# Performance work log

Measured on AMD Instinct MI355X. Metric: run time of the kernel, lower is better.

## Reference

```python
import jax, jax.numpy as jnp
import numpy as np

IN_FEATURES_LS = (64, 128, 256, 512)
OUT_FEATURES = 1024
MAX_FEAT = max(IN_FEATURES_LS)
N_TOKENS = 65536


def setup_inputs() -> dict:
    key = jax.random.key(0)
    kx, kg, kw, kb = jax.random.split(key, 4)
    x = jax.random.normal(kx, (N_TOKENS, MAX_FEAT), dtype=jnp.float32)
    gidx = jax.random.randint(kg, (N_TOKENS,), 0, len(IN_FEATURES_LS))
    # per-sample declared input size; values are exactly entries of IN_FEATURES_LS
    in_feat_size = jnp.asarray(IN_FEATURES_LS, dtype=jnp.int64 if jax.config.jax_enable_x64 else jnp.int32)[gidx]
    weight = jax.random.normal(kw, (len(IN_FEATURES_LS), OUT_FEATURES, MAX_FEAT), dtype=jnp.float32) * 0.02
    bias = jax.random.normal(kb, (len(IN_FEATURES_LS), OUT_FEATURES), dtype=jnp.float32) * 0.02
    return {"x": x, "in_feat_size": in_feat_size, "weight": weight, "bias": bias}


def reference(x, in_feat_size, weight, bias):
    # mask[g, i] = i < in_features_ls[g]; zero out padded weight columns
    sizes = jnp.asarray(IN_FEATURES_LS, dtype=jnp.int32)
    feat_mask = (jnp.arange(MAX_FEAT)[None, :] < sizes[:, None]).astype(x.dtype)  # [G, max_feat]
    out = jnp.zeros(x.shape[:-1] + (OUT_FEATURES,), dtype=x.dtype)
    for idx, feat_size in enumerate(IN_FEATURES_LS):
        w = weight[idx] * feat_mask[idx][None, :]          # [out, max_feat]
        y = jnp.einsum('oi,ni->no', w, x) + bias[idx]       # [N, out]
        sel = (in_feat_size == feat_size).astype(x.dtype)[..., None]
        out = out + sel * y
    return out
```

## Files before the change

### kernel.cpp

```cpp
#include <hip/hip_runtime.h>
#include <hip/hip_bf16.h>

#define N_TOKENS 65536
#define MAXF 512
#define OUTF 1024
#define NGROUP 4

typedef __attribute__((ext_vector_type(8))) short short8;
typedef __attribute__((ext_vector_type(4))) float floatx4;
typedef unsigned short ushort_t;
typedef unsigned int uint_t;

__device__ __forceinline__ uint_t f2bf(float f) {
    uint_t u = __float_as_uint(f);
    u += 0x7fffu + ((u >> 16) & 1u);
    return u >> 16;
}

#define OFF_BASES  0
#define OFF_BHIST  4096
#define OFF_BSTART 8192
#define OFF_LISTS  16384
#define OFF_XB     (1u<<20)
#define OFF_WB     ((1u<<20) + ((size_t)N_TOKENS*MAXF*2))
#define WS_FULL    (OFF_WB + (size_t)NGROUP*OUTF*MAXF*2)
#define WS_MIN     (OFF_LISTS + (size_t)N_TOKENS*4)

__constant__ int c_wstart[4] = {0, 65536, 196608, 458752};

__global__ void hist_kernel(const int* __restrict__ sizes, int* __restrict__ blockHist) {
    __shared__ int h[4][NGROUP];
    int t = threadIdx.x, wave = t >> 6;
    int tok = blockIdx.x * 256 + t;
    int g = __ffs(sizes[tok]) - 7;
    #pragma unroll
    for (int gg = 0; gg < NGROUP; ++gg) {
        unsigned long long m = __ballot(g == gg);
        if ((t & 63) == 0) h[wave][gg] = __popcll(m);
    }
    __syncthreads();
    if (t < NGROUP)
        blockHist[blockIdx.x * NGROUP + t] = h[0][t] + h[1][t] + h[2][t] + h[3][t];
}

__global__ void scan_kernel(const int* __restrict__ blockHist,
                            int* __restrict__ blockStart, int* __restrict__ bases) {
    __shared__ int4 sh[256];
    int t = threadIdx.x;
    int4 v = ((const int4*)blockHist)[t];
    sh[t] = v;
    __syncthreads();
    for (int d = 1; d < 256; d <<= 1) {
        int4 u = sh[t];
        int4 a = make_int4(0, 0, 0, 0);
        if (t >= d) a = sh[t - d];
        __syncthreads();
        u.x += a.x; u.y += a.y; u.z += a.z; u.w += a.w;
        sh[t] = u;
        __syncthreads();
    }
    int4 incl = sh[t];
    int4 tot = sh[255];
    int b0 = 0, b1 = tot.x, b2 = b1 + tot.y, b3 = b2 + tot.z, b4 = b3 + tot.w;
    blockStart[t * 4 + 0] = b0 + incl.x - v.x;
    blockStart[t * 4 + 1] = b1 + incl.y - v.y;
    blockStart[t * 4 + 2] = b2 + incl.z - v.z;
    blockStart[t * 4 + 3] = b3 + incl.w - v.w;
    if (t == 0) {
        bases[0] = b0; bases[1] = b1; bases[2] = b2; bases[3] = b3; bases[4] = b4;
    }
}

__global__ void scatter_kernel(const int* __restrict__ sizes,
                               const int* __restrict__ blockStart,
                               int* __restrict__ lists) {
    __shared__ int wcnt[4][NGROUP];
    int t = threadIdx.x, wave = t >> 6, lane = t & 63;
    int tok = blockIdx.x * 256 + t;
    int g = __ffs(sizes[tok]) - 7;
    int pos = 0;
    #pragma unroll
    for (int gg = 0; gg < NGROUP; ++gg) {
        unsigned long long m = __ballot(g == gg);
        if (g == gg) pos = __popcll(m & ((1ull << lane) - 1ull));
        if (lane == 0) wcnt[wave][gg] = __popcll(m);
    }
    __syncthreads();
    int off = blockStart[blockIdx.x * 4 + g];
    for (int w = 0; w < wave; ++w) off += wcnt[w][g];
    lists[off + pos] = tok;
}

__global__ void convx_kernel(const float* __restrict__ x, const int* __restrict__ bases,
                             const int* __restrict__ lists, ushort_t* __restrict__ xb) {
    int c0 = bases[1] - bases[0], c1 = bases[2] - bases[1],
        c2 = bases[3] - bases[2], c3 = bases[4] - bases[3];
    int p1 = c0 << 3;
    int p2 = p1 + (c1 << 4);
    int p3 = p2 + (c2 << 5);
    int T  = p3 + (c3 << 6);
    int xs1 = c0 << 6;
    int xs2 = xs1 + (c1 << 7);
    int xs3 = xs2 + (c2 << 8);
    int stride = gridDim.x * blockDim.x;
    for (int id = blockIdx.x * blockDim.x + threadIdx.x; id < T; id += stride) {
        int g, local, base, xs;
        if (id < p1)      { g = 0; local = id;      base = bases[0]; xs = 0;   }
        else if (id < p2) { g = 1; local = id - p1; base = bases[1]; xs = xs1; }
        else if (id < p3) { g = 2; local = id - p2; base = bases[2]; xs = xs2; }
        else              { g = 3; local = id - p3; base = bases[3]; xs = xs3; }
        int shift = 3 + g;
        int sl = local >> shift;
        int k  = (local - (sl << shift)) << 3;
        int tok = lists[base + sl];
        const floatx4* src = (const floatx4*)(x + (size_t)tok * MAXF + k);
        floatx4 a = src[0], b = src[1];
        short8 v;
        v[0] = (short)f2bf(a[0]); v[1] = (short)f2bf(a[1]);
        v[2] = (short)f2bf(a[2]); v[3] = (short)f2bf(a[3]);
        v[4] = (short)f2bf(b[0]); v[5] = (short)f2bf(b[1]);
        v[6] = (short)f2bf(b[2]); v[7] = (short)f2bf(b[3]);
        *(short8*)(xb + (size_t)xs + ((size_t)sl << (6 + g)) + k) = v;
    }
}

__global__ void convw_kernel(const float* __restrict__ weight, ushort_t* __restrict__ wb) {
    int id = blockIdx.x * 256 + threadIdx.x;
    int g, local, ws;
    if (id < 8192)       { g = 0; local = id;         ws = 0;      }
    else if (id < 24576) { g = 1; local = id - 8192;  ws = 65536;  }
    else if (id < 57344) { g = 2; local = id - 24576; ws = 196608; }
    else                 { g = 3; local = id - 57344; ws = 458752; }
    int shift = 3 + g;
    int row = local >> shift;
    int k = (local - (row << shift)) << 3;
    const floatx4* src = (const floatx4*)(weight + (size_t)g * OUTF * MAXF + (size_t)row * MAXF + k);
    floatx4 a = src[0], b = src[1];
    short8 v;
    v[0] = (short)f2bf(a[0]); v[1] = (short)f2bf(a[1]);
    v[2] = (short)f2bf(a[2]); v[3] = (short)f2bf(a[3]);
    v[4] = (short)f2bf(b[0]); v[5] = (short)f2bf(b[1]);
    v[6] = (short)f2bf(b[2]); v[7] = (short)f2bf(b[3]);
    *(short8*)(wb + ws + ((size_t)row << (6 + g)) + k) = v;
}

#define GLOAD_LDS16(gptr, lptr)                                                \
    __builtin_amdgcn_global_load_lds(                                          \
        (const __attribute__((address_space(1))) uint_t*)(gptr),               \
        (__attribute__((address_space(3))) uint_t*)(lptr), 16, 0, 0)

__global__ __launch_bounds__(512, 1) void gemm_bf16_kernel(
    const ushort_t* __restrict__ xb, const ushort_t* __restrict__ wb,
    const float* __restrict__ bias, const int* __restrict__ bases,
    const int* __restrict__ lists, float* __restrict__ out) {

    const int c0 = bases[1] - bases[0], c1 = bases[2] - bases[1],
              c2 = bases[3] - bases[2], c3 = bases[4] - bases[3];
    const int t0 = ((c0 + 255) >> 8) << 2;
    const int t1 = ((c1 + 255) >> 8) << 2;
    const int t2 = ((c2 + 255) >> 8) << 2;
    const int t3 = ((c3 + 255) >> 8) << 2;
    const int xs1 = c0 << 6;
    const int xs2 = xs1 + (c1 << 7);
    const int xs3 = xs2 + (c2 << 8);

    int id = blockIdx.x;
    int g, local, count, gbase, xs, wsb;
    if (id < t0)                { g = 0; local = id;                count = c0; gbase = bases[0]; xs = 0;   wsb = 0;      }
    else if (id < t0 + t1)      { g = 1; local = id - t0;           count = c1; gbase = bases[1]; xs = xs1; wsb = 65536;  }
    else if (id < t0 + t1 + t2) { g = 2; local = id - t0 - t1;      count = c2; gbase = bases[2]; xs = xs2; wsb = 196608; }
    else if (id < t0 + t1 + t2 + t3)
                                { g = 3; local = id - t0 - t1 - t2; count = c3; gbase = bases[3]; xs = xs3; wsb = 458752; }
    else return;

    const int mt = local >> 2, nt = local & 3;
    const int m_base = mt << 8;
    const int n_base = nt << 8;
    const int K_log = 6 + g;
    const int nsteps = 1 << (g + 1);
    const int rows = min(256, count - m_base);

    __shared__ ushort_t As[2][256 * 32];
    __shared__ ushort_t Bs[2][256 * 32];

    const int t = threadIdx.x;
    const int wave = t >> 6, lane = t & 63;
    const int wm = wave >> 2, wn = wave & 3;
    const int quad = lane >> 4, l16 = lane & 15;
    const int rsub = lane >> 2;
    const int kq   = (lane & 3) * 8;

    const ushort_t* aptr[2];
    const ushort_t* bptr[2];
    #pragma unroll
    for (int j = 0; j < 2; ++j) {
        int br = wave * 32 + j * 16;
        int ar = min(m_base + br + rsub, count - 1);
        aptr[j] = xb + (size_t)xs + ((size_t)ar << K_log) + kq;
        int nr = n_base + br + rsub;
        bptr[j] = wb + (size_t)wsb + ((size_t)nr << K_log) + kq;
    }

    floatx4 acc[8][4];
    #pragma unroll
    for (int i = 0; i < 8; ++i)
        #pragma unroll
        for (int j = 0; j < 4; ++j) acc[i][j] = (floatx4)(0.0f);

    #pragma unroll
    for (int j = 0; j < 2; ++j) {
        int br = wave * 32 + j * 16;
        GLOAD_LDS16(aptr[j], &As[0][br * 32]);
        GLOAD_LDS16(bptr[j], &Bs[0][br * 32]);
    }
    __syncthreads();

    int buf = 0;
    for (int s = 0; s < nsteps; ++s) {
        if (s + 1 < nsteps) {
            int k0 = (s + 1) << 5;
            #pragma unroll
            for (int j = 0; j < 2; ++j) {
                int br = wave * 32 + j * 16;
                GLOAD_LDS16(aptr[j] + k0, &As[buf ^ 1][br * 32]);
                GLOAD_LDS16(bptr[j] + k0, &Bs[buf ^ 1][br * 32]);
            }
        }
        short8 af[8], bf[4];
        #pragma unroll
        for (int mi = 0; mi < 8; ++mi)
            af[mi] = *(const short8*)&As[buf][(wm * 128 + mi * 16 + l16) * 32 + quad * 8];
        #pragma unroll
        for (int ni = 0; ni < 4; ++ni)
            bf[ni] = *(const short8*)&Bs[buf][(wn * 64 + ni * 16 + l16) * 32 + quad * 8];
        #pragma unroll
        for (int mi = 0; mi < 8; ++mi)
            #pragma unroll
            for (int ni = 0; ni < 4; ++ni)
                acc[mi][ni] = __builtin_amdgcn_mfma_f32_16x16x32_bf16(
                    af[mi], bf[ni], acc[mi][ni], 0, 0, 0);
        __syncthreads();
        buf ^= 1;
    }

    #pragma unroll
    for (int ni = 0; ni < 4; ++ni) {
        int col = n_base + wn * 64 + ni * 16 + l16;
        float bv = bias[g * OUTF + col];
        #pragma unroll
        for (int mi = 0; mi < 8; ++mi) {
            int mloc = wm * 128 + mi * 16 + quad * 4;
            #pragma unroll
            for (int r = 0; r < 4; ++r) {
                int m = mloc + r;
                if (m < rows) {
                    int tok = lists[gbase + m_base + m];
                    out[(size_t)tok * OUTF + col] = acc[mi][ni][r] + bv;
                }
            }
        }
    }
}

__global__ __launch_bounds__(256) void gemm_fp32_kernel(
    const float* __restrict__ x, const float* __restrict__ weight,
    const float* __restrict__ bias, const int* __restrict__ bases,
    const int* __restrict__ lists, float* __restrict__ out) {

    const int g = blockIdx.z;
    const int gbase = bases[g];
    const int count = bases[g + 1] - gbase;
    const int m_base = blockIdx.y * 128;
    if (m_base >= count) return;
    const int n_base = blockIdx.x * 128;
    const int K = 64 << g;
    const int rows = min(128, count - m_base);

    __shared__ ushort_t As[128][40];
    __shared__ ushort_t Bs[128][40];
    __shared__ int idxs[128];

    const int t = threadIdx.x;
    if (t < 128) idxs[t] = (t < rows) ? lists[gbase + m_base + t] : lists[gbase + m_base];
    __syncthreads();

    const int wave = t >> 6, lane = t & 63;
    const int wm = wave >> 1, wn = wave & 1;
    const int quad = lane >> 4, l16 = lane & 15;

    floatx4 acc[4][4];
    #pragma unroll
    for (int i = 0; i < 4; ++i)
        #pragma unroll
        for (int j = 0; j < 4; ++j) acc[i][j] = (floatx4)(0.0f);

    const float* wg = weight + (size_t)g * OUTF * MAXF;

    for (int k0 = 0; k0 < K; k0 += 32) {
        #pragma unroll
        for (int rep = 0; rep < 4; ++rep) {
            int id = t + rep * 256;
            int row = id >> 3;
            int kqq = id & 7;
            floatx4 av = *(const floatx4*)(x + (size_t)idxs[row] * MAXF + k0 + kqq * 4);
            unsigned long long pa = (unsigned long long)f2bf(av[0]) |
                ((unsigned long long)f2bf(av[1]) << 16) |
                ((unsigned long long)f2bf(av[2]) << 32) |
                ((unsigned long long)f2bf(av[3]) << 48);
            *(unsigned long long*)&As[row][kqq * 4] = pa;
            floatx4 bvv = *(const floatx4*)(wg + (size_t)(n_base + row) * MAXF + k0 + kqq * 4);
            unsigned long long pb = (unsigned long long)f2bf(bvv[0]) |
                ((unsigned long long)f2bf(bvv[1]) << 16) |
                ((unsigned long long)f2bf(bvv[2]) << 32) |
                ((unsigned long long)f2bf(bvv[3]) << 48);
            *(unsigned long long*)&Bs[row][kqq * 4] = pb;
        }
        __syncthreads();

        short8 af[4], bf[4];
        #pragma unroll
        for (int mi = 0; mi < 4; ++mi)
            af[mi] = *(const short8*)&As[wm * 64 + mi * 16 + l16][quad * 8];
        #pragma unroll
        for (int ni = 0; ni < 4; ++ni)
            bf[ni] = *(const short8*)&Bs[wn * 64 + ni * 16 + l16][quad * 8];
        #pragma unroll
        for (int mi = 0; mi < 4; ++mi)
            #pragma unroll
            for (int ni = 0; ni < 4; ++ni)
                acc[mi][ni] = __builtin_amdgcn_mfma_f32_16x16x32_bf16(
                    af[mi], bf[ni], acc[mi][ni], 0, 0, 0);
        __syncthreads();
    }

    #pragma unroll
    for (int ni = 0; ni < 4; ++ni) {
        int col = n_base + wn * 64 + ni * 16 + l16;
        float bv = bias[g * OUTF + col];
        #pragma unroll
        for (int mi = 0; mi < 4; ++mi) {
            int mloc = wm * 64 + mi * 16 + quad * 4;
            #pragma unroll
            for (int r = 0; r < 4; ++r) {
                int m = mloc + r;
                if (m < rows)
                    out[(size_t)idxs[m] * OUTF + col] = acc[mi][ni][r] + bv;
            }
        }
    }
}

extern "C" void kernel_launch(void* const* d_in, const int* in_sizes, int n_in,
                              void* d_out, int out_size, void* d_ws, size_t ws_size,
                              hipStream_t stream) {
    const float* x      = (const float*)d_in[0];
    const int*   sizes  = (const int*)d_in[1];
    const float* weight = (const float*)d_in[2];
    const float* bias   = (const float*)d_in[3];
    float* out = (float*)d_out;

    char* ws = (char*)d_ws;
    int* bases      = (int*)(ws + OFF_BASES);
    int* blockHist  = (int*)(ws + OFF_BHIST);
    int* blockStart = (int*)(ws + OFF_BSTART);
    int* lists      = (int*)(ws + OFF_LISTS);
    ushort_t* xb    = (ushort_t*)(ws + OFF_XB);
    ushort_t* wb    = (ushort_t*)(ws + OFF_WB);

    hist_kernel<<<N_TOKENS / 256, 256, 0, stream>>>(sizes, blockHist);
    scan_kernel<<<1, 256, 0, stream>>>(blockHist, blockStart, bases);
    scatter_kernel<<<N_TOKENS / 256, 256, 0, stream>>>(sizes, blockStart, lists);

    if (ws_size >= WS_FULL) {
        convw_kernel<<<480, 256, 0, stream>>>(weight, wb);
        convx_kernel<<<2048, 256, 0, stream>>>(x, bases, lists, xb);
        gemm_bf16_kernel<<<1036, 512, 0, stream>>>(xb, wb, bias, bases, lists, out);
    } else {
        dim3 grid(OUTF / 128, N_TOKENS / 128, NGROUP);
        gemm_fp32_kernel<<<grid, 256, 0, stream>>>(x, weight, bias, bases, lists, out);
    }
}
```

Before: 484.5 us.

## Merge prep kernels, fuse conversions, triple-buffer GEMM with swizzled LDS

Replaces the histogram/scan/scatter chain with one atomic-based prep kernel that writes per-group token lists at fixed offsets. The two bf16 conversion kernels become one launch. The GEMM gets a three-stage LDS ring in dynamic shared memory with explicit vmcnt waits and one barrier per step, an XOR swizzle on the LDS column to cut bank conflicts, and output token indices cached in LDS. The goal is fewer launches and better overlap of loads with MFMA, at the cost of nondeterministic list order and more shared memory per block.

```diff
diff --git a/kernel.cpp b/kernel.cpp
--- a/kernel.cpp
+++ b/kernel.cpp
@@ -17,64 +17,17 @@
     return u >> 16;
 }
 
-#define OFF_BASES  0
-#define OFF_BHIST  4096
-#define OFF_BSTART 8192
+#define OFF_CNT    0
 #define OFF_LISTS  16384
-#define OFF_XB     (1u<<20)
-#define OFF_WB     ((1u<<20) + ((size_t)N_TOKENS*MAXF*2))
+#define OFF_XB     (2u<<20)
+#define OFF_WB     ((2u<<20) + ((size_t)N_TOKENS*MAXF*2))
 #define WS_FULL    (OFF_WB + (size_t)NGROUP*OUTF*MAXF*2)
-#define WS_MIN     (OFF_LISTS + (size_t)N_TOKENS*4)
-
-__constant__ int c_wstart[4] = {0, 65536, 196608, 458752};
-
-__global__ void hist_kernel(const int* __restrict__ sizes, int* __restrict__ blockHist) {
-    __shared__ int h[4][NGROUP];
-    int t = threadIdx.x, wave = t >> 6;
-    int tok = blockIdx.x * 256 + t;
-    int g = __ffs(sizes[tok]) - 7;
-    #pragma unroll
-    for (int gg = 0; gg < NGROUP; ++gg) {
-        unsigned long long m = __ballot(g == gg);
-        if ((t & 63) == 0) h[wave][gg] = __popcll(m);
-    }
-    __syncthreads();
-    if (t < NGROUP)
-        blockHist[blockIdx.x * NGROUP + t] = h[0][t] + h[1][t] + h[2][t] + h[3][t];
-}
-
-__global__ void scan_kernel(const int* __restrict__ blockHist,
-                            int* __restrict__ blockStart, int* __restrict__ bases) {
-    __shared__ int4 sh[256];
-    int t = threadIdx.x;
-    int4 v = ((const int4*)blockHist)[t];
-    sh[t] = v;
-    __syncthreads();
-    for (int d = 1; d < 256; d <<= 1) {
-        int4 u = sh[t];
-        int4 a = make_int4(0, 0, 0, 0);
-        if (t >= d) a = sh[t - d];
-        __syncthreads();
-        u.x += a.x; u.y += a.y; u.z += a.z; u.w += a.w;
-        sh[t] = u;
-        __syncthreads();
-    }
-    int4 incl = sh[t];
-    int4 tot = sh[255];
-    int b0 = 0, b1 = tot.x, b2 = b1 + tot.y, b3 = b2 + tot.z, b4 = b3 + tot.w;
-    blockStart[t * 4 + 0] = b0 + incl.x - v.x;
-    blockStart[t * 4 + 1] = b1 + incl.y - v.y;
-    blockStart[t * 4 + 2] = b2 + incl.z - v.z;
-    blockStart[t * 4 + 3] = b3 + incl.w - v.w;
-    if (t == 0) {
-        bases[0] = b0; bases[1] = b1; bases[2] = b2; bases[3] = b3; bases[4] = b4;
-    }
-}
-
-__global__ void scatter_kernel(const int* __restrict__ sizes,
-                               const int* __restrict__ blockStart,
-                               int* __restrict__ lists) {
+#define WS_MIN     (OFF_LISTS + (size_t)NGROUP*N_TOKENS*4)
+
+__global__ void prep_kernel(const int* __restrict__ sizes, int* __restrict__ cnt,
+                            int* __restrict__ lists) {
     __shared__ int wcnt[4][NGROUP];
+    __shared__ int gbase[NGROUP];
     int t = threadIdx.x, wave = t >> 6, lane = t & 63;
     int tok = blockIdx.x * 256 + t;
     int g = __ffs(sizes[tok]) - 7;
@@ -86,62 +39,65 @@
         if (lane == 0) wcnt[wave][gg] = __popcll(m);
     }
     __syncthreads();
-    int off = blockStart[blockIdx.x * 4 + g];
+    if (t < NGROUP) {
+        int tot = wcnt[0][t] + wcnt[1][t] + wcnt[2][t] + wcnt[3][t];
+        gbase[t] = atomicAdd(&cnt[t], tot);
+    }
+    __syncthreads();
+    int off = gbase[g];
     for (int w = 0; w < wave; ++w) off += wcnt[w][g];
-    lists[off + pos] = tok;
-}
-
-__global__ void convx_kernel(const float* __restrict__ x, const int* __restrict__ bases,
-                             const int* __restrict__ lists, ushort_t* __restrict__ xb) {
-    int c0 = bases[1] - bases[0], c1 = bases[2] - bases[1],
-        c2 = bases[3] - bases[2], c3 = bases[4] - bases[3];
+    lists[(g << 16) + off + pos] = tok;
+}
+
+__global__ void conv_kernel(const float* __restrict__ x, const float* __restrict__ weight,
+                            const int* __restrict__ cnt, const int* __restrict__ lists,
+                            ushort_t* __restrict__ xb, ushort_t* __restrict__ wb) {
+    int c0 = cnt[0], c1 = cnt[1], c2 = cnt[2], c3 = cnt[3];
     int p1 = c0 << 3;
     int p2 = p1 + (c1 << 4);
     int p3 = p2 + (c2 << 5);
-    int T  = p3 + (c3 << 6);
+    int xT = p3 + (c3 << 6);
+    int T = 122880 + xT;
     int xs1 = c0 << 6;
     int xs2 = xs1 + (c1 << 7);
     int xs3 = xs2 + (c2 << 8);
     int stride = gridDim.x * blockDim.x;
     for (int id = blockIdx.x * blockDim.x + threadIdx.x; id < T; id += stride) {
-        int g, local, base, xs;
-        if (id < p1)      { g = 0; local = id;      base = bases[0]; xs = 0;   }
-        else if (id < p2) { g = 1; local = id - p1; base = bases[1]; xs = xs1; }
-        else if (id < p3) { g = 2; local = id - p2; base = bases[2]; xs = xs2; }
-        else              { g = 3; local = id - p3; base = bases[3]; xs = xs3; }
-        int shift = 3 + g;
-        int sl = local >> shift;
-        int k  = (local - (sl << shift)) << 3;
-        int tok = lists[base + sl];
-        const floatx4* src = (const floatx4*)(x + (size_t)tok * MAXF + k);
+        const floatx4* src;
+        ushort_t* dst;
+        if (id < 122880) {
+            int g, local, wsb;
+            if (id < 8192)       { g = 0; local = id;         wsb = 0;      }
+            else if (id < 24576) { g = 1; local = id - 8192;  wsb = 65536;  }
+            else if (id < 57344) { g = 2; local = id - 24576; wsb = 196608; }
+            else                 { g = 3; local = id - 57344; wsb = 458752; }
+            int shift = 3 + g;
+            int row = local >> shift;
+            int k = (local - (row << shift)) << 3;
+            src = (const floatx4*)(weight + (size_t)g * OUTF * MAXF + (size_t)row * MAXF + k);
+            dst = wb + wsb + ((size_t)row << (6 + g)) + k;
+        } else {
+            int xid = id - 122880;
+            int g, local, xs;
+            if (xid < p1)      { g = 0; local = xid;      xs = 0;   }
+            else if (xid < p2) { g = 1; local = xid - p1; xs = xs1; }
+            else if (xid < p3) { g = 2; local = xid - p2; xs = xs2; }
+            else               { g = 3; local = xid - p3; xs = xs3; }
+            int shift = 3 + g;
+            int sl = local >> shift;
+            int k = (local - (sl << shift)) << 3;
+            int tok = lists[(g << 16) + sl];
+            src = (const floatx4*)(x + (size_t)tok * MAXF + k);
+            dst = xb + (size_t)xs + ((size_t)sl << (6 + g)) + k;
+        }
         floatx4 a = src[0], b = src[1];
         short8 v;
         v[0] = (short)f2bf(a[0]); v[1] = (short)f2bf(a[1]);
         v[2] = (short)f2bf(a[2]); v[3] = (short)f2bf(a[3]);
         v[4] = (short)f2bf(b[0]); v[5] = (short)f2bf(b[1]);
         v[6] = (short)f2bf(b[2]); v[7] = (short)f2bf(b[3]);
-        *(short8*)(xb + (size_t)xs + ((size_t)sl << (6 + g)) + k) = v;
-    }
-}
-
-__global__ void convw_kernel(const float* __restrict__ weight, ushort_t* __restrict__ wb) {
-    int id = blockIdx.x * 256 + threadIdx.x;
-    int g, local, ws;
-    if (id < 8192)       { g = 0; local = id;         ws = 0;      }
-    else if (id < 24576) { g = 1; local = id - 8192;  ws = 65536;  }
-    else if (id < 57344) { g = 2; local = id - 24576; ws = 196608; }
-    else                 { g = 3; local = id - 57344; ws = 458752; }
-    int shift = 3 + g;
-    int row = local >> shift;
-    int k = (local - (row << shift)) << 3;
-    const floatx4* src = (const floatx4*)(weight + (size_t)g * OUTF * MAXF + (size_t)row * MAXF + k);
-    floatx4 a = src[0], b = src[1];
-    short8 v;
-    v[0] = (short)f2bf(a[0]); v[1] = (short)f2bf(a[1]);
-    v[2] = (short)f2bf(a[2]); v[3] = (short)f2bf(a[3]);
-    v[4] = (short)f2bf(b[0]); v[5] = (short)f2bf(b[1]);
-    v[6] = (short)f2bf(b[2]); v[7] = (short)f2bf(b[3]);
-    *(short8*)(wb + ws + ((size_t)row << (6 + g)) + k) = v;
+        *(short8*)dst = v;
+    }
 }
 
 #define GLOAD_LDS16(gptr, lptr)                                                \
@@ -151,11 +107,12 @@
 
 __global__ __launch_bounds__(512, 1) void gemm_bf16_kernel(
     const ushort_t* __restrict__ xb, const ushort_t* __restrict__ wb,
-    const float* __restrict__ bias, const int* __restrict__ bases,
+    const float* __restrict__ bias, const int* __restrict__ cnt,
     const int* __restrict__ lists, float* __restrict__ out) {
 
-    const int c0 = bases[1] - bases[0], c1 = bases[2] - bases[1],
-              c2 = bases[3] - bases[2], c3 = bases[4] - bases[3];
+    extern __shared__ char sh[];
+
+    const int c0 = cnt[0], c1 = cnt[1], c2 = cnt[2], c3 = cnt[3];
     const int t0 = ((c0 + 255) >> 8) << 2;
     const int t1 = ((c1 + 255) >> 8) << 2;
     const int t2 = ((c2 + 255) >> 8) << 2;
@@ -165,12 +122,12 @@
     const int xs3 = xs2 + (c2 << 8);
 
     int id = blockIdx.x;
-    int g, local, count, gbase, xs, wsb;
-    if (id < t0)                { g = 0; local = id;                count = c0; gbase = bases[0]; xs = 0;   wsb = 0;      }
-    else if (id < t0 + t1)      { g = 1; local = id - t0;           count = c1; gbase = bases[1]; xs = xs1; wsb = 65536;  }
-    else if (id < t0 + t1 + t2) { g = 2; local = id - t0 - t1;      count = c2; gbase = bases[2]; xs = xs2; wsb = 196608; }
+    int g, local, count, xs, wsb;
+    if (id < t0)                { g = 0; local = id;                count = c0; xs = 0;   wsb = 0;      }
+    else if (id < t0 + t1)      { g = 1; local = id - t0;           count = c1; xs = xs1; wsb = 65536;  }
+    else if (id < t0 + t1 + t2) { g = 2; local = id - t0 - t1;      count = c2; xs = xs2; wsb = 196608; }
     else if (id < t0 + t1 + t2 + t3)
-                                { g = 3; local = id - t0 - t1 - t2; count = c3; gbase = bases[3]; xs = xs3; wsb = 458752; }
+                                { g = 3; local = id - t0 - t1 - t2; count = c3; xs = xs3; wsb = 458752; }
     else return;
 
     const int mt = local >> 2, nt = local & 3;
@@ -180,15 +137,20 @@
     const int nsteps = 1 << (g + 1);
     const int rows = min(256, count - m_base);
 
-    __shared__ ushort_t As[2][256 * 32];
-    __shared__ ushort_t Bs[2][256 * 32];
-
     const int t = threadIdx.x;
     const int wave = t >> 6, lane = t & 63;
     const int wm = wave >> 2, wn = wave & 3;
     const int quad = lane >> 4, l16 = lane & 15;
     const int rsub = lane >> 2;
-    const int kq   = (lane & 3) * 8;
+    const int kq = (((lane & 3) ^ ((lane >> 3) & 3)) << 3);
+    const int rp = (l16 >> 1) & 3;
+
+    int* oidx = (int*)(sh + 98304);
+
+    if (t < 256) {
+        int m = m_base + t;
+        oidx[t] = (m < count) ? lists[(g << 16) + m] : 0;
+    }
 
     const ushort_t* aptr[2];
     const ushort_t* bptr[2];
@@ -197,8 +159,7 @@
         int br = wave * 32 + j * 16;
         int ar = min(m_base + br + rsub, count - 1);
         aptr[j] = xb + (size_t)xs + ((size_t)ar << K_log) + kq;
-        int nr = n_base + br + rsub;
-        bptr[j] = wb + (size_t)wsb + ((size_t)nr << K_log) + kq;
+        bptr[j] = wb + (size_t)wsb + ((size_t)(n_base + br + rsub) << K_log) + kq;
     }
 
     floatx4 acc[8][4];
@@ -210,37 +171,56 @@
     #pragma unroll
     for (int j = 0; j < 2; ++j) {
         int br = wave * 32 + j * 16;
-        GLOAD_LDS16(aptr[j], &As[0][br * 32]);
-        GLOAD_LDS16(bptr[j], &Bs[0][br * 32]);
-    }
-    __syncthreads();
+        GLOAD_LDS16(aptr[j], sh + br * 64);
+        GLOAD_LDS16(bptr[j], sh + 16384 + br * 64);
+    }
+    if (nsteps > 1) {
+        #pragma unroll
+        for (int j = 0; j < 2; ++j) {
+            int br = wave * 32 + j * 16;
+            GLOAD_LDS16(aptr[j] + 32, sh + 32768 + br * 64);
+            GLOAD_LDS16(bptr[j] + 32, sh + 32768 + 16384 + br * 64);
+        }
+    }
 
     int buf = 0;
     for (int s = 0; s < nsteps; ++s) {
-        if (s + 1 < nsteps) {
-            int k0 = (s + 1) << 5;
+        if (s + 1 < nsteps)
+            asm volatile("s_waitcnt vmcnt(4) lgkmcnt(0)" ::: "memory");
+        else
+            asm volatile("s_waitcnt vmcnt(0) lgkmcnt(0)" ::: "memory");
+        __builtin_amdgcn_s_barrier();
+        asm volatile("" ::: "memory");
+
+        const ushort_t* Ab = (const ushort_t*)(sh + buf * 32768);
+        const ushort_t* Bb = (const ushort_t*)(sh + buf * 32768 + 16384);
+        short8 af[8], bfr[4];
+        #pragma unroll
+        for (int mi = 0; mi < 8; ++mi)
+            af[mi] = *(const short8*)&Ab[(wm * 128 + mi * 16 + l16) * 32 + ((quad ^ rp) << 3)];
+        #pragma unroll
+        for (int ni = 0; ni < 4; ++ni)
+            bfr[ni] = *(const short8*)&Bb[(wn * 64 + ni * 16 + l16) * 32 + ((quad ^ rp) << 3)];
+
+        #pragma unroll
+        for (int mi = 0; mi < 8; ++mi)
+            #pragma unroll
+            for (int ni = 0; ni < 4; ++ni)
+                acc[mi][ni] = __builtin_amdgcn_mfma_f32_16x16x32_bf16(
+                    af[mi], bfr[ni], acc[mi][ni], 0, 0, 0);
+
+        if (s + 2 < nsteps) {
+            int k0 = (s + 2) << 5;
+            int bn = buf + 2; if (bn >= 3) bn -= 3;
+            char* dstA = sh + bn * 32768;
             #pragma unroll
             for (int j = 0; j < 2; ++j) {
                 int br = wave * 32 + j * 16;
-                GLOAD_LDS16(aptr[j] + k0, &As[buf ^ 1][br * 32]);
-                GLOAD_LDS16(bptr[j] + k0, &Bs[buf ^ 1][br * 32]);
+                GLOAD_LDS16(aptr[j] + k0, dstA + br * 64);
+                GLOAD_LDS16(bptr[j] + k0, dstA + 16384 + br * 64);
             }
         }
-        short8 af[8], bf[4];
-        #pragma unroll
-        for (int mi = 0; mi < 8; ++mi)
-            af[mi] = *(const short8*)&As[buf][(wm * 128 + mi * 16 + l16) * 32 + quad * 8];
-        #pragma unroll
-        for (int ni = 0; ni < 4; ++ni)
-            bf[ni] = *(const short8*)&Bs[buf][(wn * 64 + ni * 16 + l16) * 32 + quad * 8];
-        #pragma unroll
-        for (int mi = 0; mi < 8; ++mi)
-            #pragma unroll
-            for (int ni = 0; ni < 4; ++ni)
-                acc[mi][ni] = __builtin_amdgcn_mfma_f32_16x16x32_bf16(
-                    af[mi], bf[ni], acc[mi][ni], 0, 0, 0);
-        __syncthreads();
-        buf ^= 1;
+        buf = (buf == 2) ? 0 : buf + 1;
     }
 
     #pragma unroll
@@ -253,10 +233,8 @@
             #pragma unroll
             for (int r = 0; r < 4; ++r) {
                 int m = mloc + r;
-                if (m < rows) {
-                    int tok = lists[gbase + m_base + m];
-                    out[(size_t)tok * OUTF + col] = acc[mi][ni][r] + bv;
-                }
+                if (m < rows)
+                    out[(size_t)oidx[m] * OUTF + col] = acc[mi][ni][r] + bv;
             }
         }
     }
@@ -264,12 +242,11 @@
 
 __global__ __launch_bounds__(256) void gemm_fp32_kernel(
     const float* __restrict__ x, const float* __restrict__ weight,
-    const float* __restrict__ bias, const int* __restrict__ bases,
+    const float* __restrict__ bias, const int* __restrict__ cnt,
     const int* __restrict__ lists, float* __restrict__ out) {
 
     const int g = blockIdx.z;
-    const int gbase = bases[g];
-    const int count = bases[g + 1] - gbase;
+    const int count = cnt[g];
     const int m_base = blockIdx.y * 128;
     if (m_base >= count) return;
     const int n_base = blockIdx.x * 128;
@@ -281,7 +258,8 @@
     __shared__ int idxs[128];
 
     const int t = threadIdx.x;
-    if (t < 128) idxs[t] = (t < rows) ? lists[gbase + m_base + t] : lists[gbase + m_base];
+    if (t < 128) idxs[t] = (t < rows) ? lists[(g << 16) + m_base + t]
+                                      : lists[(g << 16) + m_base];
     __syncthreads();
 
     const int wave = t >> 6, lane = t & 63;
@@ -317,19 +295,19 @@
         }
         __syncthreads();
 
-        short8 af[4], bf[4];
+        short8 af[4], bfr[4];
         #pragma unroll
         for (int mi = 0; mi < 4; ++mi)
             af[mi] = *(const short8*)&As[wm * 64 + mi * 16 + l16][quad * 8];
         #pragma unroll
         for (int ni = 0; ni < 4; ++ni)
-            bf[ni] = *(const short8*)&Bs[wn * 64 + ni * 16 + l16][quad * 8];
+            bfr[ni] = *(const short8*)&Bs[wn * 64 + ni * 16 + l16][quad * 8];
         #pragma unroll
         for (int mi = 0; mi < 4; ++mi)
             #pragma unroll
             for (int ni = 0; ni < 4; ++ni)
                 acc[mi][ni] = __builtin_amdgcn_mfma_f32_16x16x32_bf16(
-                    af[mi], bf[ni], acc[mi][ni], 0, 0, 0);
+                    af[mi], bfr[ni], acc[mi][ni], 0, 0, 0);
         __syncthreads();
     }
 
@@ -360,23 +338,25 @@
     float* out = (float*)d_out;
 
     char* ws = (char*)d_ws;
-    int* bases      = (int*)(ws + OFF_BASES);
-    int* blockHist  = (int*)(ws + OFF_BHIST);
-    int* blockStart = (int*)(ws + OFF_BSTART);
-    int* lists      = (int*)(ws + OFF_LISTS);
-    ushort_t* xb    = (ushort_t*)(ws + OFF_XB);
-    ushort_t* wb    = (ushort_t*)(ws + OFF_WB);
-
-    hist_kernel<<<N_TOKENS / 256, 256, 0, stream>>>(sizes, blockHist);
-    scan_kernel<<<1, 256, 0, stream>>>(blockHist, blockStart, bases);
-    scatter_kernel<<<N_TOKENS / 256, 256, 0, stream>>>(sizes, blockStart, lists);
+    int* cnt   = (int*)(ws + OFF_CNT);
+    int* lists = (int*)(ws + OFF_LISTS);
+    ushort_t* xb = (ushort_t*)(ws + OFF_XB);
+    ushort_t* wb = (ushort_t*)(ws + OFF_WB);
+
+    hipMemsetAsync(ws + OFF_CNT, 0, NGROUP * sizeof(int), stream);
+    prep_kernel<<<N_TOKENS / 256, 256, 0, stream>>>(sizes, cnt, lists);
 
     if (ws_size >= WS_FULL) {
-        convw_kernel<<<480, 256, 0, stream>>>(weight, wb);
-        convx_kernel<<<2048, 256, 0, stream>>>(x, bases, lists, xb);
-        gemm_bf16_kernel<<<1036, 512, 0, stream>>>(xb, wb, bias, bases, lists, out);
+        static int attr_done = 0;
+        if (!attr_done) {
+            hipFuncSetAttribute((const void*)gemm_bf16_kernel,
+                                hipFuncAttributeMaxDynamicSharedMemorySize, 99328);
+            attr_done = 1;
+        }
+        conv_kernel<<<2048, 256, 0, stream>>>(x, weight, cnt, lists, xb, wb);
+        gemm_bf16_kernel<<<1036, 512, 99328, stream>>>(xb, wb, bias, cnt, lists, out);
     } else {
         dim3 grid(OUTF / 128, N_TOKENS / 128, NGROUP);
-        gemm_fp32_kernel<<<grid, 256, 0, stream>>>(x, weight, bias, bases, lists, out);
-    }
-}
+        gemm_fp32_kernel<<<grid, 256, 0, stream>>>(x, weight, bias, cnt, lists, out);
+    }
+}
```

Result: no change. 475.7 us (-1.8%).
